# Kernel tuning notes

Measured on AMD Instinct MI355X. Metric: run time of the kernel, lower is better.

The kernel has to match this reference:

```python
import jax, jax.numpy as jnp
import numpy as np

N_NODES = 100000


def gcn_conv(x, W, b, src, dst):
    """PyG-style GCNConv: symmetric normalization with self-loops.
    x: [N, Cin], W: [Cin, Cout], b: [Cout], src/dst: [E] int (messages src->dst)."""
    N = x.shape[0]
    h = x @ W  # [N, Cout]
    # degree with self-loops (fill_value = 1)
    deg = jnp.ones((N,), dtype=x.dtype).at[dst].add(1.0)
    d_inv = jax.lax.rsqrt(deg)
    norm = d_inv[src] * d_inv[dst]  # [E]
    msg = h[src] * norm[:, None]  # [E, Cout] -- dominant memory traffic
    agg = jnp.zeros_like(h).at[dst].add(msg)
    # self-loop contribution: norm_ii = d_inv[i]^2
    agg = agg + h * (d_inv * d_inv)[:, None]
    return agg + b


def setup_inputs() -> dict:
    key = jax.random.key(0)
    k1, k2, k3, k4 = jax.random.split(key, 4)
    N, E, Cin, Chid, Cout = N_NODES, 1600000, 128, 128, 64
    x = jax.random.normal(k1, (N, Cin), dtype=jnp.float32)
    edge_index = jax.random.randint(k2, (2, E), 0, N, dtype=jnp.int32)
    W1 = jax.random.normal(k3, (Cin, Chid), dtype=jnp.float32) / np.sqrt(Cin)
    b1 = jnp.zeros((Chid,), dtype=jnp.float32)
    W2 = jax.random.normal(k4, (Chid, Cout), dtype=jnp.float32) / np.sqrt(Chid)
    b2 = jnp.zeros((Cout,), dtype=jnp.float32)
    return {"x": x, "edge_index": edge_index, "W1": W1, "b1": b1, "W2": W2, "b2": b2}


def reference(x, edge_index, W1, b1, W2, b2):
    src, dst = edge_index[0], edge_index[1]
    h = jax.nn.relu(gcn_conv(x, W1, b1, src, dst))  # conv1: in -> 2*out
    z = jax.nn.relu(gcn_conv(h, W2, b2, src, dst))  # conv2: 2*out -> out
    return z
```

## Files before the change

### kernel.cpp

```cpp
#include <hip/hip_runtime.h>
#include <hip/hip_fp16.h>

#define TPB 256
#define CAP 40
#define OVFCAP 65536

typedef __attribute__((ext_vector_type(8))) short bf16x8;
typedef __attribute__((ext_vector_type(4))) float f32x4;

__device__ inline void split1(float x, unsigned short& h, unsigned short& l) {
  unsigned xb = __float_as_uint(x);
  h = (unsigned short)(xb >> 16);
  float hf = __uint_as_float(xb & 0xFFFF0000u);
  float lf = x - hf;
  l = (unsigned short)(__float_as_uint(lf) >> 16);
}

__device__ inline void split4(const float4 v, ushort4& h, ushort4& l) {
  split1(v.x, h.x, l.x);
  split1(v.y, h.y, l.y);
  split1(v.z, h.z, l.z);
  split1(v.w, h.w, l.w);
}

__global__ void k_fillslot(const int* __restrict__ src, const int* __restrict__ dst,
                           int* __restrict__ cnt, int* __restrict__ col2,
                           uint2* __restrict__ ovf, int* __restrict__ ovfn,
                           int E, int N) {
  const int g = blockIdx.x & 7;
  const int gb = blockIdx.x >> 3;
  const int gstride = (gridDim.x >> 3) * blockDim.x;
  const int lo = (int)(((long long)g * N) >> 3);
  const int hi = (int)(((long long)(g + 1) * N) >> 3);
  for (int e = gb * blockDim.x + threadIdx.x; e < E; e += gstride) {
    int d = __builtin_nontemporal_load(dst + e);
    if (d >= lo && d < hi) {
      int s = __builtin_nontemporal_load(src + e);
      int c = atomicAdd(cnt + d, 1);
      if (c < CAP) {
        col2[(size_t)d * CAP + c] = s;
      } else {
        int p = atomicAdd(ovfn, 1);
        if (p < OVFCAP) ovf[p] = make_uint2((unsigned)d, (unsigned)s);
      }
    }
  }
}

__global__ void k_dinv_from_cnt(const int* __restrict__ cnt, float* __restrict__ dinv, int N) {
  int i = blockIdx.x * blockDim.x + threadIdx.x;
  if (i < N) dinv[i] = rsqrtf((float)(cnt[i] + 1));
}

__global__ void k_prep_wt(const float* __restrict__ W, unsigned short* __restrict__ Wh,
                          unsigned short* __restrict__ Wl, int K, int C) {
  int i = blockIdx.x * blockDim.x + threadIdx.x;
  if (i >= K * C) return;
  int k = i / C, c = i % C;
  unsigned short h, l;
  split1(W[i], h, l);
  Wh[(size_t)c * K + k] = h;
  Wl[(size_t)c * K + k] = l;
}

template<int COUT>
__launch_bounds__(512)
__global__ void k_gemm_mfma(const float* __restrict__ X, const unsigned short* __restrict__ Wh,
                            const unsigned short* __restrict__ Wl, const float* __restrict__ dinv,
                            __half* __restrict__ Y16, int N) {
  constexpr int K = 128;
  constexpr int BM = 128;
  constexpr int WCOL = COUT / 2;
  constexpr int NFRAG = WCOL / 16;
  __shared__ unsigned short Ah[BM * K], Al[BM * K];
  __shared__ unsigned short Wsh[COUT * K], Wsl[COUT * K];

  const int tid = threadIdx.x;
  const int rb = blockIdx.x * BM;

  {
    const uint4* gh = (const uint4*)Wh;
    const uint4* gl = (const uint4*)Wl;
    for (int i = tid; i < COUT * 16; i += 512) {
      int r = i >> 4, c = i & 15;
      int byte = r * 256 + ((c * 16) ^ ((r & 7) << 4));
      *(uint4*)((char*)Wsh + byte) = gh[i];
      *(uint4*)((char*)Wsl + byte) = gl[i];
    }
  }
  {
    for (int i = tid; i < BM * 32; i += 512) {
      int r = i >> 5, c4 = i & 31;
      int g = rb + r;
      if (g < N) {
        float4 v = ((const float4*)(X + (size_t)g * K))[c4];
        ushort4 h, l;
        split4(v, h, l);
        int byte = r * 256 + ((c4 * 8) ^ ((r & 7) << 4));
        *(ushort4*)((char*)Ah + byte) = h;
        *(ushort4*)((char*)Al + byte) = l;
      }
    }
  }
  __syncthreads();

  const int wid = tid >> 6, lane = tid & 63;
  const int wm = wid & 3;
  const int wn = wid >> 2;
  const int RB = wm * 32;
  const int CB = wn * WCOL;
  const int l15 = lane & 15, l4 = lane >> 4;
  const int xs = (l15 & 7) << 4;

  f32x4 acc[2][NFRAG];
  #pragma unroll
  for (int m = 0; m < 2; ++m)
    #pragma unroll
    for (int n = 0; n < NFRAG; ++n)
      acc[m][n] = (f32x4){0.f, 0.f, 0.f, 0.f};

  #pragma unroll
  for (int ks = 0; ks < 4; ++ks) {
    const int cbx = (ks * 64 + l4 * 16) ^ xs;
    bf16x8 a0h = *(const bf16x8*)((const char*)Ah + (RB + l15) * 256 + cbx);
    bf16x8 a0l = *(const bf16x8*)((const char*)Al + (RB + l15) * 256 + cbx);
    bf16x8 a1h = *(const bf16x8*)((const char*)Ah + (RB + 16 + l15) * 256 + cbx);
    bf16x8 a1l = *(const bf16x8*)((const char*)Al + (RB + 16 + l15) * 256 + cbx);
    #pragma unroll
    for (int n = 0; n < NFRAG; ++n) {
      const int wr = CB + n * 16 + l15;
      bf16x8 bh = *(const bf16x8*)((const char*)Wsh + wr * 256 + cbx);
      bf16x8 bl = *(const bf16x8*)((const char*)Wsl + wr * 256 + cbx);
      acc[0][n] = __builtin_amdgcn_mfma_f32_16x16x32_bf16(a0h, bh, acc[0][n], 0, 0, 0);
      acc[0][n] = __builtin_amdgcn_mfma_f32_16x16x32_bf16(a0h, bl, acc[0][n], 0, 0, 0);
      acc[0][n] = __builtin_amdgcn_mfma_f32_16x16x32_bf16(a0l, bh, acc[0][n], 0, 0, 0);
      acc[1][n] = __builtin_amdgcn_mfma_f32_16x16x32_bf16(a1h, bh, acc[1][n], 0, 0, 0);
      acc[1][n] = __builtin_amdgcn_mfma_f32_16x16x32_bf16(a1h, bl, acc[1][n], 0, 0, 0);
      acc[1][n] = __builtin_amdgcn_mfma_f32_16x16x32_bf16(a1l, bh, acc[1][n], 0, 0, 0);
    }
  }

  #pragma unroll
  for (int m = 0; m < 2; ++m) {
    #pragma unroll
    for (int q = 0; q < 4; ++q) {
      int row = rb + RB + m * 16 + l4 * 4 + q;
      if (row < N) {
        float dv = dinv[row];
        __half* yr = Y16 + (size_t)row * COUT + CB + l15;
        #pragma unroll
        for (int n = 0; n < NFRAG; ++n) yr[n * 16] = __float2half(acc[m][n][q] * dv);
      }
    }
  }
}

template<int C>
__launch_bounds__(256)
__global__ void k_aggv(const __half* __restrict__ hsh, const float* __restrict__ dinv,
                       const int* __restrict__ cnt, const int* __restrict__ col2,
                       const uint2* __restrict__ ovf, const int* __restrict__ ovfn,
                       const float* __restrict__ bias, float* __restrict__ out, int N) {
  constexpr int LPR = C / 8;
  constexpr int NG = 64 / LPR;
  const int node = blockIdx.x * 4 + (threadIdx.x >> 6);
  if (node >= N) return;
  const int lane = threadIdx.x & 63;
  const int i = lane % LPR;
  const int j = lane / LPR;
  const int deg = cnt[node];
  const int m = min(deg, CAP);
  const int* cp = col2 + (size_t)node * CAP;
  const size_t coloff = (size_t)i * 8;

  float acc[8];
  #pragma unroll
  for (int q = 0; q < 8; ++q) acc[q] = 0.f;

  for (int k = 0; k < m; k += 2 * NG) {
    int s0 = k + j, s1 = k + NG + j;
    bool ok0 = s0 < m, ok1 = s1 < m;
    int n0 = cp[ok0 ? s0 : m - 1];
    int n1 = cp[ok1 ? s1 : m - 1];
    uint4 v0 = *(const uint4*)((const char*)hsh + ((size_t)n0 * C + coloff) * 2);
    uint4 v1 = *(const uint4*)((const char*)hsh + ((size_t)n1 * C + coloff) * 2);
    float f0 = ok0 ? 1.f : 0.f;
    float f1 = ok1 ? 1.f : 0.f;
    const __half2* h0 = (const __half2*)&v0;
    const __half2* h1 = (const __half2*)&v1;
    #pragma unroll
    for (int q = 0; q < 4; ++q) {
      float2 a = __half22float2(h0[q]);
      float2 b = __half22float2(h1[q]);
      acc[2 * q]     = fmaf(f0, a.x, acc[2 * q]);
      acc[2 * q + 1] = fmaf(f0, a.y, acc[2 * q + 1]);
      acc[2 * q]     = fmaf(f1, b.x, acc[2 * q]);
      acc[2 * q + 1] = fmaf(f1, b.y, acc[2 * q + 1]);
    }
  }

  if (deg > CAP && j == 0) {
    int on = min(*ovfn, (int)OVFCAP);
    for (int k = 0; k < on; ++k) {
      uint2 eo = ovf[k];
      if ((int)eo.x == node) {
        uint4 v = *(const uint4*)((const char*)hsh + ((size_t)eo.y * C + coloff) * 2);
        const __half2* h2 = (const __half2*)&v;
        #pragma unroll
        for (int q = 0; q < 4; ++q) {
          float2 a = __half22float2(h2[q]);
          acc[2 * q] += a.x;
          acc[2 * q + 1] += a.y;
        }
      }
    }
  }

  #pragma unroll
  for (int off = LPR; off < 64; off <<= 1)
    #pragma unroll
    for (int q = 0; q < 8; ++q)
      acc[q] += __shfl_xor(acc[q], off);

  if (j < 2) {
    const float dv = dinv[node];
    const int f4 = 2 * i + j;
    uint2 sh = *(const uint2*)((const char*)hsh + ((size_t)node * C + (size_t)f4 * 4) * 2);
    const __half2* shh = (const __half2*)&sh;
    float2 s01 = __half22float2(shh[0]);
    float2 s23 = __half22float2(shh[1]);
    float4 bb = ((const float4*)bias)[f4];
    float4 o;
    o.x = fmaxf(fmaf(dv, s01.x + acc[4 * j + 0], bb.x), 0.f);
    o.y = fmaxf(fmaf(dv, s01.y + acc[4 * j + 1], bb.y), 0.f);
    o.z = fmaxf(fmaf(dv, s23.x + acc[4 * j + 2], bb.z), 0.f);
    o.w = fmaxf(fmaf(dv, s23.y + acc[4 * j + 3], bb.w), 0.f);
    ((float4*)(out + (size_t)node * C))[f4] = o;
  }
}

__global__ void k_fill1(float* __restrict__ p, int n) {
  int i = blockIdx.x * blockDim.x + threadIdx.x;
  if (i < n) p[i] = 1.0f;
}
__global__ void k_deg_scatter(const int* __restrict__ dst, float* __restrict__ deg, int E) {
  int e = blockIdx.x * blockDim.x + threadIdx.x;
  if (e < E) atomicAdd(deg + dst[e], 1.0f);
}
__global__ void k_rsqrt_inplace(float* __restrict__ p, int n) {
  int i = blockIdx.x * blockDim.x + threadIdx.x;
  if (i < n) p[i] = rsqrtf(p[i]);
}
template<int COUT>
__launch_bounds__(256)
__global__ void k_gemm128(const float* __restrict__ X, const float* __restrict__ W,
                          const float* __restrict__ dinv, float* __restrict__ Y, int N) {
  constexpr int K = 128;
  constexpr int CG = COUT / 8;
  constexpr int ROWS = 256 / CG;
  constexpr int XSTR = K + 4;
  __shared__ float Ws[K * COUT];
  __shared__ float Xs[ROWS * XSTR];
  const int tid = threadIdx.x;

  const float4* W4 = (const float4*)W;
  float4* Ws4 = (float4*)Ws;
  #pragma unroll
  for (int i = tid; i < K * COUT / 4; i += 256) Ws4[i] = W4[i];

  const int rb = blockIdx.x * ROWS;
  float4* Xs4 = (float4*)Xs;
  for (int i = tid; i < ROWS * (K / 4); i += 256) {
    int r = i / (K / 4), c = i % (K / 4);
    float4 v = make_float4(0.f, 0.f, 0.f, 0.f);
    if (rb + r < N) v = ((const float4*)(X + (size_t)(rb + r) * K))[c];
    Xs4[r * (XSTR / 4) + c] = v;
  }
  __syncthreads();

  const int lrow = tid / CG;
  const int cg = tid % CG;
  const int row = rb + lrow;
  float acc[8];
  #pragma unroll
  for (int jj = 0; jj < 8; ++jj) acc[jj] = 0.f;
  const float* xr = Xs + lrow * XSTR;
  #pragma unroll 4
  for (int k = 0; k < K; ++k) {
    float xv = xr[k];
    float4 w0 = Ws4[k * (COUT / 4) + cg * 2];
    float4 w1 = Ws4[k * (COUT / 4) + cg * 2 + 1];
    acc[0] = fmaf(xv, w0.x, acc[0]);
    acc[1] = fmaf(xv, w0.y, acc[1]);
    acc[2] = fmaf(xv, w0.z, acc[2]);
    acc[3] = fmaf(xv, w0.w, acc[3]);
    acc[4] = fmaf(xv, w1.x, acc[4]);
    acc[5] = fmaf(xv, w1.y, acc[5]);
    acc[6] = fmaf(xv, w1.z, acc[6]);
    acc[7] = fmaf(xv, w1.w, acc[7]);
  }
  if (row < N) {
    float ds = dinv[row];
    float4* y = (float4*)(Y + (size_t)row * COUT + cg * 8);
    y[0] = make_float4(acc[0] * ds, acc[1] * ds, acc[2] * ds, acc[3] * ds);
    y[1] = make_float4(acc[4] * ds, acc[5] * ds, acc[6] * ds, acc[7] * ds);
  }
}
template<int C>
__global__ void k_selfinit2(const float* __restrict__ hs, const float* __restrict__ dinv,
                            float* __restrict__ agg, int N) {
  int i = blockIdx.x * blockDim.x + threadIdx.x;
  int total = N * (C / 4);
  if (i >= total) return;
  int node = i / (C / 4);
  float di = dinv[node];
  float4 v = ((const float4*)hs)[i];
  ((float4*)agg)[i] = make_float4(v.x * di, v.y * di, v.z * di, v.w * di);
}
template<int C>
__global__ void k_scatter(const float* __restrict__ hs, const float* __restrict__ dinv,
                          const int* __restrict__ src, const int* __restrict__ dst,
                          float* __restrict__ agg, int E) {
  constexpr int LPE = C / 4;
  long long t = (long long)blockIdx.x * blockDim.x + threadIdx.x;
  int e = (int)(t / LPE);
  if (e >= E) return;
  int c4 = (int)(t % LPE);
  int s = src[e], d = dst[e];
  float nd = dinv[d];
  float4 v = ((const float4*)(hs + (size_t)s * C))[c4];
  float* a = agg + (size_t)d * C + (size_t)c4 * 4;
  atomicAdd(a + 0, v.x * nd);
  atomicAdd(a + 1, v.y * nd);
  atomicAdd(a + 2, v.z * nd);
  atomicAdd(a + 3, v.w * nd);
}
template<int C>
__global__ void k_relu_bias(const float* __restrict__ agg, const float* __restrict__ b,
                            float* __restrict__ out, int N) {
  int i = blockIdx.x * blockDim.x + threadIdx.x;
  int total = N * (C / 4);
  if (i >= total) return;
  int c4 = i % (C / 4);
  float4 bb = ((const float4*)b)[c4];
  float4 v = ((const float4*)agg)[i];
  v.x = fmaxf(v.x + bb.x, 0.f);
  v.y = fmaxf(v.y + bb.y, 0.f);
  v.z = fmaxf(v.z + bb.z, 0.f);
  v.w = fmaxf(v.w + bb.w, 0.f);
  ((float4*)out)[i] = v;
}

extern "C" void kernel_launch(void* const* d_in, const int* in_sizes, int n_in,
                              void* d_out, int out_size, void* d_ws, size_t ws_size,
                              hipStream_t stream) {
  const float* x  = (const float*)d_in[0];
  const int*   ei = (const int*)d_in[1];
  const float* W1 = (const float*)d_in[2];
  const float* b1 = (const float*)d_in[3];
  const float* W2 = (const float*)d_in[4];
  const float* b2 = (const float*)d_in[5];

  const int Cin = 128, Chid = 128, Cout2 = 64;
  const int N = in_sizes[0] / Cin;
  const int E = in_sizes[1] / 2;
  const int* src = ei;
  const int* dst = ei + E;
  float* out = (float*)d_out;
  (void)n_in; (void)out_size;

  const int nbN = (N + TPB - 1) / TPB;
  const int nbE = (E + TPB - 1) / TPB;

  auto align = [](size_t v) { return (v + 511) & ~(size_t)511; };
  char* ws = (char*)d_ws;
  size_t off = 0;
  float* dinv   = (float*)(ws + off); off += align((size_t)N * 4);
  int*   cnt    = (int*)(ws + off);   off += align((size_t)N * 4);
  unsigned short* wt1h = (unsigned short*)(ws + off); off += align((size_t)Cin * Chid * 2);
  unsigned short* wt1l = (unsigned short*)(ws + off); off += align((size_t)Cin * Chid * 2);
  unsigned short* wt2h = (unsigned short*)(ws + off); off += align((size_t)Chid * Cout2 * 2);
  unsigned short* wt2l = (unsigned short*)(ws + off); off += align((size_t)Chid * Cout2 * 2);
  int*   col2   = (int*)(ws + off);   off += align((size_t)N * CAP * 4);
  int*   ovfn   = (int*)(ws + off);   off += align((size_t)64);
  uint2* ovf    = (uint2*)(ws + off); off += align((size_t)OVFCAP * 8);
  float* B      = (float*)(ws + off); off += (size_t)N * Chid * 4;
  __half* H16   = (__half*)(ws + off); off += align((size_t)N * Chid * 2);

  const bool fast_ok = (off <= ws_size);

  if (fast_ok) {
    hipMemsetAsync(cnt, 0, (size_t)N * 4, stream);
    hipMemsetAsync(ovfn, 0, 4, stream);
    k_fillslot<<<2048, TPB, 0, stream>>>(src, dst, cnt, col2, ovf, ovfn, E, N);
    k_dinv_from_cnt<<<nbN, TPB, 0, stream>>>(cnt, dinv, N);

    k_prep_wt<<<(Cin * Chid + TPB - 1) / TPB, TPB, 0, stream>>>(W1, wt1h, wt1l, Cin, Chid);
    k_prep_wt<<<(Chid * Cout2 + TPB - 1) / TPB, TPB, 0, stream>>>(W2, wt2h, wt2l, Chid, Cout2);

    k_gemm_mfma<128><<<(N + 127) / 128, 512, 0, stream>>>(x, wt1h, wt1l, dinv, H16, N);
    k_aggv<128><<<(N + 3) / 4, 256, 0, stream>>>(H16, dinv, cnt, col2, ovf, ovfn, b1, B, N);
    k_gemm_mfma<64><<<(N + 127) / 128, 512, 0, stream>>>(B, wt2h, wt2l, dinv, H16, N);
    k_aggv<64><<<(N + 3) / 4, 256, 0, stream>>>(H16, dinv, cnt, col2, ovf, ovfn, b2, out, N);
  } else {
    size_t o2 = 0;
    float* dinvF = (float*)(ws + o2); o2 += align((size_t)N * 4);
    float* AF = (float*)(ws + o2);    o2 += (size_t)N * Chid * 4;
    float* BF = (float*)(ws + o2);

    k_fill1<<<nbN, TPB, 0, stream>>>(dinvF, N);
    k_deg_scatter<<<nbE, TPB, 0, stream>>>(dst, dinvF, E);
    k_rsqrt_inplace<<<nbN, TPB, 0, stream>>>(dinvF, N);

    k_gemm128<128><<<(N + 15) / 16, 256, 0, stream>>>(x, W1, dinvF, AF, N);
    k_selfinit2<128><<<(N * 32 + TPB - 1) / TPB, TPB, 0, stream>>>(AF, dinvF, BF, N);
    {
      long long total = (long long)E * 32;
      k_scatter<128><<<(int)((total + TPB - 1) / TPB), TPB, 0, stream>>>(AF, dinvF, src, dst, BF, E);
    }
    k_relu_bias<128><<<(N * 32 + TPB - 1) / TPB, TPB, 0, stream>>>(BF, b1, AF, N);

    k_gemm128<64><<<(N + 31) / 32, 256, 0, stream>>>(AF, W2, dinvF, BF, N);
    k_selfinit2<64><<<(N * 16 + TPB - 1) / TPB, TPB, 0, stream>>>(BF, dinvF, out, N);
    {
      long long total = (long long)E * 16;
      k_scatter<64><<<(int)((total + TPB - 1) / TPB), TPB, 0, stream>>>(BF, dinvF, src, dst, out, E);
    }
    k_relu_bias<64><<<(N * 16 + TPB - 1) / TPB, TPB, 0, stream>>>(out, b2, out, N);
  }
}
```

Before: 264.9 us.

## Merge weight-prep kernels, unroll gather loop by four, double fillslot grid

The two weight split/transpose kernels are fused into one launch, which removes a kernel launch. The neighbor-gather loop in the aggregation kernel now handles four neighbor rows per iteration instead of two, so more memory loads are in flight at once. The edge slot-filling kernel gets twice as many blocks. The wider unroll raises register use and wastes more masked loads on low-degree nodes.

```diff
diff --git a/kernel.cpp b/kernel.cpp
--- a/kernel.cpp
+++ b/kernel.cpp
@@ -52,15 +52,26 @@
   if (i < N) dinv[i] = rsqrtf((float)(cnt[i] + 1));
 }
 
-__global__ void k_prep_wt(const float* __restrict__ W, unsigned short* __restrict__ Wh,
-                          unsigned short* __restrict__ Wl, int K, int C) {
-  int i = blockIdx.x * blockDim.x + threadIdx.x;
-  if (i >= K * C) return;
-  int k = i / C, c = i % C;
-  unsigned short h, l;
-  split1(W[i], h, l);
-  Wh[(size_t)c * K + k] = h;
-  Wl[(size_t)c * K + k] = l;
+__global__ void k_prep_wt2(const float* __restrict__ W1, unsigned short* __restrict__ W1h,
+                           unsigned short* __restrict__ W1l, int K1, int C1,
+                           const float* __restrict__ W2, unsigned short* __restrict__ W2h,
+                           unsigned short* __restrict__ W2l, int K2, int C2) {
+  int i = blockIdx.x * blockDim.x + threadIdx.x;
+  int n1 = K1 * C1;
+  if (i < n1) {
+    int k = i / C1, c = i % C1;
+    unsigned short h, l;
+    split1(W1[i], h, l);
+    W1h[(size_t)c * K1 + k] = h;
+    W1l[(size_t)c * K1 + k] = l;
+  } else if (i < n1 + K2 * C2) {
+    int ii = i - n1;
+    int k = ii / C2, c = ii % C2;
+    unsigned short h, l;
+    split1(W2[ii], h, l);
+    W2h[(size_t)c * K2 + k] = h;
+    W2l[(size_t)c * K2 + k] = l;
+  }
 }
 
 template<int COUT>
@@ -177,25 +188,37 @@
   #pragma unroll
   for (int q = 0; q < 8; ++q) acc[q] = 0.f;
 
-  for (int k = 0; k < m; k += 2 * NG) {
-    int s0 = k + j, s1 = k + NG + j;
-    bool ok0 = s0 < m, ok1 = s1 < m;
+  for (int k = 0; k < m; k += 4 * NG) {
+    int s0 = k + j, s1 = k + NG + j, s2 = k + 2 * NG + j, s3 = k + 3 * NG + j;
+    bool ok0 = s0 < m, ok1 = s1 < m, ok2 = s2 < m, ok3 = s3 < m;
     int n0 = cp[ok0 ? s0 : m - 1];
     int n1 = cp[ok1 ? s1 : m - 1];
+    int n2 = cp[ok2 ? s2 : m - 1];
+    int n3 = cp[ok3 ? s3 : m - 1];
     uint4 v0 = *(const uint4*)((const char*)hsh + ((size_t)n0 * C + coloff) * 2);
     uint4 v1 = *(const uint4*)((const char*)hsh + ((size_t)n1 * C + coloff) * 2);
-    float f0 = ok0 ? 1.f : 0.f;
-    float f1 = ok1 ? 1.f : 0.f;
+    uint4 v2 = *(const uint4*)((const char*)hsh + ((size_t)n2 * C + coloff) * 2);
+    uint4 v3 = *(const uint4*)((const char*)hsh + ((size_t)n3 * C + coloff) * 2);
+    float f0 = ok0 ? 1.f : 0.f, f1 = ok1 ? 1.f : 0.f;
+    float f2 = ok2 ? 1.f : 0.f, f3 = ok3 ? 1.f : 0.f;
     const __half2* h0 = (const __half2*)&v0;
     const __half2* h1 = (const __half2*)&v1;
+    const __half2* h2 = (const __half2*)&v2;
+    const __half2* h3 = (const __half2*)&v3;
     #pragma unroll
     for (int q = 0; q < 4; ++q) {
       float2 a = __half22float2(h0[q]);
       float2 b = __half22float2(h1[q]);
+      float2 c = __half22float2(h2[q]);
+      float2 d = __half22float2(h3[q]);
       acc[2 * q]     = fmaf(f0, a.x, acc[2 * q]);
       acc[2 * q + 1] = fmaf(f0, a.y, acc[2 * q + 1]);
       acc[2 * q]     = fmaf(f1, b.x, acc[2 * q]);
       acc[2 * q + 1] = fmaf(f1, b.y, acc[2 * q + 1]);
+      acc[2 * q]     = fmaf(f2, c.x, acc[2 * q]);
+      acc[2 * q + 1] = fmaf(f2, c.y, acc[2 * q + 1]);
+      acc[2 * q]     = fmaf(f3, d.x, acc[2 * q]);
+      acc[2 * q + 1] = fmaf(f3, d.y, acc[2 * q + 1]);
     }
   }
 
@@ -392,11 +415,14 @@
   if (fast_ok) {
     hipMemsetAsync(cnt, 0, (size_t)N * 4, stream);
     hipMemsetAsync(ovfn, 0, 4, stream);
-    k_fillslot<<<2048, TPB, 0, stream>>>(src, dst, cnt, col2, ovf, ovfn, E, N);
+    k_fillslot<<<4096, TPB, 0, stream>>>(src, dst, cnt, col2, ovf, ovfn, E, N);
     k_dinv_from_cnt<<<nbN, TPB, 0, stream>>>(cnt, dinv, N);
 
-    k_prep_wt<<<(Cin * Chid + TPB - 1) / TPB, TPB, 0, stream>>>(W1, wt1h, wt1l, Cin, Chid);
-    k_prep_wt<<<(Chid * Cout2 + TPB - 1) / TPB, TPB, 0, stream>>>(W2, wt2h, wt2l, Chid, Cout2);
+    {
+      int total = Cin * Chid + Chid * Cout2;
+      k_prep_wt2<<<(total + TPB - 1) / TPB, TPB, 0, stream>>>(
+          W1, wt1h, wt1l, Cin, Chid, W2, wt2h, wt2l, Chid, Cout2);
+    }
 
     k_gemm_mfma<128><<<(N + 127) / 128, 512, 0, stream>>>(x, wt1h, wt1l, dinv, H16, N);
     k_aggv<128><<<(N + 3) / 4, 256, 0, stream>>>(H16, dinv, cnt, col2, ovf, ovfn, b1, B, N);
```

Result: faster. 256.1 us (-3.3%).
